# Performance work log

Measured on AMD Instinct MI355X. Metric: run time of the kernel, lower is better.

The kernel has to match this reference:

```python
import jax, jax.numpy as jnp
import numpy as np

D_MODEL = 2048
N_HEADS = 16
D_K = D_MODEL // N_HEADS
BATCH = 4
SEQ = 2048


def setup_inputs() -> dict:
    key = jax.random.key(0)
    ks = jax.random.split(key, 9)
    s = 1.0 / np.sqrt(D_MODEL)
    return {
        "x": jax.random.normal(ks[0], (BATCH, SEQ, D_MODEL), dtype=jnp.float32),
        "wq_w": jax.random.normal(ks[1], (D_MODEL, D_MODEL), dtype=jnp.float32) * s,
        "wq_b": jax.random.normal(ks[2], (D_MODEL,), dtype=jnp.float32) * 0.02,
        "wk_w": jax.random.normal(ks[3], (D_MODEL, D_MODEL), dtype=jnp.float32) * s,
        "wk_b": jax.random.normal(ks[4], (D_MODEL,), dtype=jnp.float32) * 0.02,
        "wv_w": jax.random.normal(ks[5], (D_MODEL, D_MODEL), dtype=jnp.float32) * s,
        "wv_b": jax.random.normal(ks[6], (D_MODEL,), dtype=jnp.float32) * 0.02,
        "wo_w": jax.random.normal(ks[7], (D_MODEL, D_MODEL), dtype=jnp.float32) * s,
        "wo_b": jax.random.normal(ks[8], (D_MODEL,), dtype=jnp.float32) * 0.02,
    }


def reference(x, wq_w, wq_b, wk_w, wk_b, wv_w, wv_b, wo_w, wo_b):
    b, s, _ = x.shape
    # Linear projections (torch Linear: x @ W^T + b)
    def split_heads(t):  # (b, s, d_model) -> (b, h, s, d_k)
        return t.reshape(b, s, N_HEADS, D_K).transpose(0, 2, 1, 3)
    q = split_heads(x @ wq_w.T + wq_b)
    k = split_heads(x @ wk_w.T + wk_b)
    v = split_heads(x @ wv_w.T + wv_b)
    scale = 1.0 / jnp.sqrt(jnp.asarray(D_K, dtype=x.dtype))
    scores = jnp.einsum("bhqd,bhkd->bhqk", q, k) * scale  # (b, h, s, s)
    attn = jax.nn.softmax(scores, axis=-1)
    ctx = jnp.einsum("bhqk,bhkd->bhqd", attn, v)
    ctx = ctx.transpose(0, 2, 1, 3).reshape(b, s, D_MODEL)
    out = ctx @ wo_w.T + wo_b
    return out
```

## Files before the change

kernel.cpp:

```cpp
#include <hip/hip_runtime.h>
#include <hip/hip_bf16.h>
#include <math.h>

typedef __attribute__((ext_vector_type(8))) short short8;
typedef __attribute__((ext_vector_type(4))) float f32x4;
typedef __attribute__((ext_vector_type(16))) float f32x16;
typedef __attribute__((ext_vector_type(4))) unsigned short u16x4;
typedef __attribute__((ext_vector_type(8))) unsigned short u16x8;
typedef __attribute__((ext_vector_type(4))) unsigned int u32x4;
typedef __attribute__((ext_vector_type(2))) int i32x2;
typedef unsigned short u16;
typedef unsigned int u32;

#define DM 2048
#define SQ 2048
#define NB 4
#define NH 16
#define DKH 128
#define KT 64
#define NT (SQ / KT)
#define LD3 (3 * DM)
#define QSCALE (0.08838834764831845f * 1.4426950408889634f)

__device__ __forceinline__ u16 f2bf(float f) {
  unsigned u = __float_as_uint(f);
  u += 0x7fffu + ((u >> 16) & 1u);
  return (u16)(u >> 16);
}

__device__ __forceinline__ u32 cvtpk(float lo, float hi) {
  u32 r;
  asm("v_cvt_pk_bf16_f32 %0, %1, %2" : "=v"(r) : "v"(lo), "v"(hi));
  return r;
}

__device__ __forceinline__ void gload16(const u16* g, u16* lds) {
  __builtin_amdgcn_global_load_lds(
      (const __attribute__((address_space(1))) unsigned int*)g,
      (__attribute__((address_space(3))) unsigned int*)lds, 16, 0, 0);
}

__device__ __forceinline__ int paddr16(int r, int k, int nkt) {
  const int cid = (((r >> 8) * nkt + (k >> 6)) << 5) | (((r >> 7) & 1) << 4) |
                  (((r >> 5) & 3) << 2) | ((k >> 4) & 3);
  return (cid << 9) + (((r & 31) | (((k >> 3) & 1) << 5)) << 3) + (k & 7);
}

__global__ void cvt_x_p(const float* __restrict__ in, u16* __restrict__ out) {
  const int idx = blockIdx.x * 256 + threadIdx.x;
  const int r = idx >> 8;
  const int k = (idx & 255) << 3;
  const float4 v0 = *(const float4*)(in + (size_t)r * DM + k);
  const float4 v1 = *(const float4*)(in + (size_t)r * DM + k + 4);
  u16x8 o;
  o[0] = f2bf(v0.x); o[1] = f2bf(v0.y); o[2] = f2bf(v0.z); o[3] = f2bf(v0.w);
  o[4] = f2bf(v1.x); o[5] = f2bf(v1.y); o[6] = f2bf(v1.z); o[7] = f2bf(v1.w);
  *(u16x8*)(out + paddr16(r, k, 32)) = o;
}

__global__ void cvt_w_p(const float* __restrict__ w0, const float* __restrict__ w1,
                        const float* __restrict__ w2, const float* __restrict__ w3,
                        u16* __restrict__ dq, u16* __restrict__ dw) {
  const int sel = blockIdx.y;
  const float* src;
  switch (sel) {
    case 0: src = w0; break;
    case 1: src = w1; break;
    case 2: src = w2; break;
    default: src = w3; break;
  }
  const int idx = blockIdx.x * 256 + threadIdx.x;
  const int r = idx >> 8;
  const int k = (idx & 255) << 3;
  const float4 v0 = *(const float4*)(src + (size_t)r * DM + k);
  const float4 v1 = *(const float4*)(src + (size_t)r * DM + k + 4);
  u16x8 o;
  o[0] = f2bf(v0.x); o[1] = f2bf(v0.y); o[2] = f2bf(v0.z); o[3] = f2bf(v0.w);
  o[4] = f2bf(v1.x); o[5] = f2bf(v1.y); o[6] = f2bf(v1.z); o[7] = f2bf(v1.w);
  if (sel < 3)
    *(u16x8*)(dq + paddr16(sel * DM + r, k, 32)) = o;
  else
    *(u16x8*)(dw + paddr16(r, k, 32)) = o;
}


#define STG_A(T, HALF)                                                       \
  do {                                                                       \
    _Pragma("unroll") for (int uu = 0; uu < 2; ++uu) {                       \
      const int j_ = w * 2 + uu;                                             \
      gload16(As + ((((T) * 32 + (HALF) * 16 + j_) << 9) + l * 8),           \
              &smA[((T) & 1) * 16384 + ((HALF) * 16 + j_) * 512]);           \
    }                                                                        \
  } while (0)

#define STG_B(T, HALF)                                                       \
  do {                                                                       \
    _Pragma("unroll") for (int uu = 0; uu < 2; ++uu) {                       \
      const int j_ = w * 2 + uu;                                             \
      gload16(Bs + ((((T) * 32 + (HALF) * 16 + j_) << 9) + l * 8),           \
              &smB[((T) & 1) * 16384 + ((HALF) * 16 + j_) * 512]);           \
    }                                                                        \
  } while (0)

#define LDA(QM)                                                            \
  do {                                                                     \
    const int rb_ = wr * 4 + (QM) * 2;                                     \
    const u16* p_ = &smA[bi * 16384 + rb_ * 2048 + l * 8];                 \
    _Pragma("unroll") for (int s = 0; s < 4; ++s) {                        \
      af[0][s] = *(const short8*)&p_[s * 512];                             \
      af[1][s] = *(const short8*)&p_[2048 + s * 512];                      \
    }                                                                      \
  } while (0)

#define LDB(QN)                                                            \
  do {                                                                     \
    const int rb_ = wc * 2 + (QN);                                         \
    const u16* p_ = &smB[bi * 16384 + rb_ * 2048 + l * 8];                 \
    _Pragma("unroll") for (int s = 0; s < 4; ++s)                          \
      bf[QN][s] = *(const short8*)&p_[s * 512];                            \
  } while (0)

#define MFMA_Q(QM, QN)                                                             \
  __builtin_amdgcn_s_setprio(1);                                                   \
  _Pragma("unroll") for (int s = 0; s < 4; ++s) {                                  \
    acc[(QM) * 2][(QN)] = __builtin_amdgcn_mfma_f32_32x32x16_bf16(                 \
        af[0][s], bf[QN][s], acc[(QM) * 2][(QN)], 0, 0, 0);                        \
    acc[(QM) * 2 + 1][(QN)] = __builtin_amdgcn_mfma_f32_32x32x16_bf16(             \
        af[1][s], bf[QN][s], acc[(QM) * 2 + 1][(QN)], 0, 0, 0);                    \
  }                                                                                \
  __builtin_amdgcn_s_setprio(0);

#define WAIT_LGKM                                         \
  asm volatile("s_waitcnt lgkmcnt(0)" ::: "memory");      \
  __builtin_amdgcn_sched_barrier(0);

template <int MODE>
__global__ __launch_bounds__(512, 2) void gemm8p(
    const u16* __restrict__ A, const u16* __restrict__ B,
    const float* __restrict__ bq, const float* __restrict__ bk,
    const float* __restrict__ bvp, void* __restrict__ Cout,
    int M, int N, int K) {
  __shared__ u16 smA[2 * 16384];
  __shared__ u16 smB[2 * 16384];
  const int tid = threadIdx.x;
  const int w = tid >> 6, l = tid & 63;
  const int c5 = l & 31, hi = l >> 5;
  const int wr = w >> 2, wc = w & 3;

  int flat = blockIdx.x + (int)gridDim.x * (int)blockIdx.y;
  const int nwg = (int)(gridDim.x * gridDim.y);
  flat = (flat & 7) * (nwg >> 3) + (flat >> 3);
  const int m0 = (flat / (int)gridDim.x) * 256, n0 = (flat % (int)gridDim.x) * 256;

  const int NSTEP = K / 64;
  f32x16 acc[4][2] = {};

  const u16* As = A + (size_t)(m0 >> 8) * NSTEP * 16384;
  const u16* Bs = B + (size_t)(n0 >> 8) * NSTEP * 16384;

  STG_A(0, 0); STG_A(0, 1); STG_B(0, 0); STG_B(0, 1);
  STG_B(1, 0); STG_A(1, 0);
  asm volatile("s_waitcnt vmcnt(4)" ::: "memory");
  __builtin_amdgcn_s_barrier();

  short8 af[2][4], bf[2][4];
  for (int t = 0; t < NSTEP; ++t) {
    const int bi = t & 1;
    LDA(0); LDB(0);
    if (t + 1 < NSTEP) STG_B(t + 1, 1);
    __builtin_amdgcn_s_barrier();
    WAIT_LGKM;
    MFMA_Q(0, 0);
    __builtin_amdgcn_s_barrier();
    LDB(1);
    if (t + 1 < NSTEP) STG_A(t + 1, 1);
    __builtin_amdgcn_s_barrier();
    WAIT_LGKM;
    MFMA_Q(0, 1);
    __builtin_amdgcn_s_barrier();
    LDA(1);
    if (t + 2 < NSTEP) STG_B(t + 2, 0);
    __builtin_amdgcn_s_barrier();
    WAIT_LGKM;
    MFMA_Q(1, 1);
    __builtin_amdgcn_s_barrier();
    if (t + 2 < NSTEP) STG_A(t + 2, 0);
    __builtin_amdgcn_s_barrier();
    MFMA_Q(1, 0);
    if (t + 2 < NSTEP)
      asm volatile("s_waitcnt vmcnt(4)" ::: "memory");
    else if (t + 1 < NSTEP)
      asm volatile("s_waitcnt vmcnt(0)" ::: "memory");
    __builtin_amdgcn_s_barrier();
  }

#pragma unroll
  for (int nf = 0; nf < 2; ++nf) {
    const int col = n0 + wc * 64 + nf * 32 + c5;
    float bval, os;
    if (MODE == 0) {
      const int seg = col >> 11;
      const float* bp = seg == 0 ? bq : (seg == 1 ? bk : bvp);
      bval = bp[col & (DM - 1)];
      os = (seg == 0) ? QSCALE : 1.0f;
    } else {
      bval = bq[col];
      os = 1.0f;
    }
#pragma unroll
    for (int mf = 0; mf < 4; ++mf) {
#pragma unroll
      for (int r = 0; r < 16; ++r) {
        const int row = m0 + wr * 128 + mf * 32 + (r & 3) + 8 * (r >> 2) + 4 * hi;
        const float v = (acc[mf][nf][r] + bval) * os;
        if (MODE == 1)
          ((float*)Cout)[(size_t)row * N + col] = v;
        else
          ((u16*)Cout)[(size_t)row * N + col] = f2bf(v);
      }
    }
  }
}

__global__ __launch_bounds__(512, 2) void attn(
    const u16* __restrict__ QKV, u16* __restrict__ O) {
  __shared__ u16 smK[2 * 8192];
  __shared__ u16 smV[9216];
  __shared__ float alScr[8 * 32];

  const u16* Qp = QKV;
  const u16* Kp = QKV + DM;
  const u16* Vp = QKV + 2 * DM;

  const int tid = threadIdx.x;
  const int w = tid >> 6, l = tid & 63;
  const int c5 = l & 31, hi = l >> 5;

  int flat = blockIdx.x + ((int)blockIdx.y << 3) + ((int)blockIdx.z << 7);
  flat = (flat & 7) * 64 + (flat >> 3);
  const int qt = flat & 7, h = (flat >> 3) & 15, b = flat >> 7;

  const int q0 = qt * 256 + w * 32;
  const size_t rowb = (size_t)b * SQ;
  const int hoff = h * DKH;

  short8 qf[8];
#pragma unroll
  for (int ds = 0; ds < 8; ++ds)
    qf[ds] = *(const short8*)&Qp[(rowb + q0 + c5) * LD3 + hoff + ds * 16 + hi * 8];

  f32x16 o[4] = {};
  float mrow = -1e30f, lsum = 0.f;

  const int vdg = tid >> 5;
  const int kvp = (tid & 31) * 2;
  u16x8 va, vb;

  {
#pragma unroll
    for (int uu = 0; uu < 2; ++uu) {
      const int u = w * 2 + uu;
      const int row = u * 4 + (l >> 4);
      const int col16 = (l & 15) ^ (row & 15);
      gload16(&Kp[(rowb + row) * LD3 + hoff + col16 * 8], &smK[u * 512]);
    }
    const u16* vp = &Vp[(rowb + kvp) * LD3 + hoff + vdg * 8];
    va = *(const u16x8*)vp;
    vb = *(const u16x8*)(vp + LD3);
#pragma unroll
    for (int i = 0; i < 8; ++i) {
      const int d = vdg * 8 + i;
      *(u32*)&smV[d * 72 + kvp] = (u32)va[i] | ((u32)vb[i] << 16);
    }
  }
  __syncthreads();

  int buf = 0;
  for (int t = 0; t < NT; ++t) {
    const int nb = buf ^ 1;
    if (t + 1 < NT) {
      const size_t kvr = rowb + (size_t)(t + 1) * KT;
#pragma unroll
      for (int uu = 0; uu < 2; ++uu) {
        const int u = w * 2 + uu;
        const int row = u * 4 + (l >> 4);
        const int col16 = (l & 15) ^ (row & 15);
        gload16(&Kp[(kvr + row) * LD3 + hoff + col16 * 8], &smK[nb * 8192 + u * 512]);
      }
      const u16* vp = &Vp[(kvr + kvp) * LD3 + hoff + vdg * 8];
      va = *(const u16x8*)vp;
      vb = *(const u16x8*)(vp + LD3);
    }

    f32x16 s[2] = {};
    __builtin_amdgcn_s_setprio(1);
#pragma unroll
    for (int ni = 0; ni < 2; ++ni) {
      const int row = ni * 32 + c5;
#pragma unroll
      for (int ds = 0; ds < 8; ++ds) {
        const short8 kf = *(const short8*)&smK[buf * 8192 + row * 128 + (((ds << 1) | hi) ^ (row & 15)) * 8];
        s[ni] = __builtin_amdgcn_mfma_f32_32x32x16_bf16(kf, qf[ds], s[ni], 0, 0, 0);
      }
    }
    __builtin_amdgcn_s_setprio(0);

    float mx = s[0][0];
#pragma unroll
    for (int ni = 0; ni < 2; ++ni)
#pragma unroll
      for (int i = 0; i < 16; ++i)
        mx = fmaxf(mx, s[ni][i]);
    i32x2 sw = __builtin_amdgcn_permlane32_swap(__float_as_int(mx), __float_as_int(mx), false, false);
    const float gmax = fmaxf(__int_as_float(sw.x), __int_as_float(sw.y));

    if (__any(gmax > mrow + 10.0f)) {
      const float mn = fmaxf(mrow, gmax);
      const float al = exp2f(mrow - mn);
      mrow = mn;
      lsum *= al;
      alScr[w * 32 + c5] = al;
#pragma unroll
      for (int r = 0; r < 16; ++r) {
        const float av = alScr[w * 32 + (r & 3) + 8 * (r >> 2) + 4 * hi];
#pragma unroll
        for (int dg = 0; dg < 4; ++dg) o[dg][r] *= av;
      }
    }

    float ps0 = 0.f, ps1 = 0.f;
#pragma unroll
    for (int i = 0; i < 16; ++i) {
      const float p0 = exp2f(s[0][i] - mrow);
      const float p1 = exp2f(s[1][i] - mrow);
      s[0][i] = p0; s[1][i] = p1;
      ps0 += p0; ps1 += p1;
    }
    lsum += ps0 + ps1;

    __builtin_amdgcn_s_setprio(1);
#pragma unroll
    for (int ks = 0; ks < 4; ++ks) {
      const int b0 = (ks & 1) * 8;
      const int ni = ks >> 1;
      const u32 A0 = cvtpk(s[ni][b0 + 0], s[ni][b0 + 1]);
      const u32 A1 = cvtpk(s[ni][b0 + 4], s[ni][b0 + 5]);
      const u32 B0 = cvtpk(s[ni][b0 + 2], s[ni][b0 + 3]);
      const u32 B1 = cvtpk(s[ni][b0 + 6], s[ni][b0 + 7]);
      const i32x2 r0 = __builtin_amdgcn_permlane32_swap((int)A0, (int)A1, false, false);
      const i32x2 r1 = __builtin_amdgcn_permlane32_swap((int)B0, (int)B1, false, false);
      u32x4 paw;
      paw.x = (u32)r0.x; paw.y = (u32)r1.x; paw.z = (u32)r0.y; paw.w = (u32)r1.y;
      const short8 pa = *(const short8*)&paw;
#pragma unroll
      for (int dg = 0; dg < 4; ++dg) {
        const int rowd = dg * 32 + c5;
        const short8 vf = *(const short8*)&smV[rowd * 72 + ks * 16 + hi * 8];
        o[dg] = __builtin_amdgcn_mfma_f32_32x32x16_bf16(pa, vf, o[dg], 0, 0, 0);
      }
    }
    __builtin_amdgcn_s_setprio(0);

    __syncthreads();
    if (t + 1 < NT) {
#pragma unroll
      for (int i = 0; i < 8; ++i) {
        const int d = vdg * 8 + i;
        *(u32*)&smV[d * 72 + kvp] = (u32)va[i] | ((u32)vb[i] << 16);
      }
      __syncthreads();
    }
    buf = nb;
  }

  {
    const i32x2 sl = __builtin_amdgcn_permlane32_swap(__float_as_int(lsum), __float_as_int(lsum), false, false);
    const float tot = __int_as_float(sl.x) + __int_as_float(sl.y);
    alScr[w * 32 + c5] = 1.0f / tot;
  }
#pragma unroll
  for (int r = 0; r < 16; ++r) {
    const int qloc = (r & 3) + 8 * (r >> 2) + 4 * hi;
    const float inv = alScr[w * 32 + qloc];
    const int rowg = (int)rowb + q0 + qloc;
#pragma unroll
    for (int dg = 0; dg < 4; ++dg)
      O[paddr16(rowg, hoff + dg * 32 + c5, 32)] = f2bf(o[dg][r] * inv);
  }
}

extern "C" void kernel_launch(void* const* d_in, const int* in_sizes, int n_in,
                              void* d_out, int out_size, void* d_ws, size_t ws_size,
                              hipStream_t stream) {
  const float* x    = (const float*)d_in[0];
  const float* wq_w = (const float*)d_in[1];
  const float* wq_b = (const float*)d_in[2];
  const float* wk_w = (const float*)d_in[3];
  const float* wk_b = (const float*)d_in[4];
  const float* wv_w = (const float*)d_in[5];
  const float* wv_b = (const float*)d_in[6];
  const float* wo_w = (const float*)d_in[7];
  const float* wo_b = (const float*)d_in[8];
  float* out = (float*)d_out;

  u16* p = (u16*)d_ws;
  u16* xb  = p; p += (size_t)NB * SQ * DM;
  u16* wqb = p; p += (size_t)3 * DM * DM;
  u16* wob = p; p += (size_t)DM * DM;
  u16* QKV = p; p += (size_t)NB * SQ * 3 * DM;
  u16* ctx = xb;

  cvt_x_p<<<dim3(NB * SQ * DM / 2048), dim3(256), 0, stream>>>(x, xb);
  cvt_w_p<<<dim3(DM * DM / 2048, 4), dim3(256), 0, stream>>>(wq_w, wk_w, wv_w, wo_w, wqb, wob);

  dim3 gg3(3 * DM / 256, (NB * SQ) / 256);
  gemm8p<0><<<gg3, dim3(512), 0, stream>>>(xb, wqb, wq_b, wk_b, wv_b, QKV,
                                           NB * SQ, 3 * DM, DM);

  attn<<<dim3(SQ / 256, NH, NB), dim3(512), 0, stream>>>(QKV, ctx);

  dim3 ggo(DM / 256, (NB * SQ) / 256);
  gemm8p<1><<<ggo, dim3(512), 0, stream>>>(ctx, wob, wo_b, nullptr, nullptr, out,
                                           NB * SQ, DM, DM);
}
```

Before: 587.7 us.

## Drop redundant GEMM barriers, coalesce bf16 pack writes, tree-reduce attention row max

The GEMM main loop loses the extra workgroup barriers and the explicit lgkmcnt(0) waits placed before each MFMA quarter. The compiler now places LDS waits itself, and the MFMAs can overlap with the LDS fragment loads and the async global-to-LDS staging. The fp32-to-bf16 packing kernels now iterate over the packed output index and invert the mapping with a new helper. That gives contiguous, coalesced stores at the cost of scattered reads. In attention, the QK^T loop order is swapped so the two independent MFMA chains interleave, and the row max uses a tree reduction instead of a serial chain. The risk is an LDS hazard if a removed barrier was actually guarding reuse of a staging buffer.

```diff
diff --git a/kernel.cpp b/kernel.cpp
--- a/kernel.cpp
+++ b/kernel.cpp
@@ -43,19 +43,28 @@
 __device__ __forceinline__ int paddr16(int r, int k, int nkt) {
   const int cid = (((r >> 8) * nkt + (k >> 6)) << 5) | (((r >> 7) & 1) << 4) |
                   (((r >> 5) & 3) << 2) | ((k >> 4) & 3);
-  return (cid << 9) + (((r & 31) | (((k >> 3) & 1) << 5)) << 3) + (k & 7);
+  return (cid << 9) + (((r & 31) | (((k >> 3) & 1) << 3 << 2)) << 3) + (k & 7);
+}
+
+__device__ __forceinline__ void pinv(int idx, int nkt, int& r, int& k) {
+  const int e8 = idx & 63;
+  const int cid = idx >> 6;
+  const int kt = (cid >> 5) % nkt;
+  const int rt = (cid >> 5) / nkt;
+  r = (rt << 8) + (((cid >> 4) & 1) << 7) + (((cid >> 2) & 3) << 5) + (e8 & 31);
+  k = (kt << 6) + ((cid & 3) << 4) + ((e8 >> 5) << 3);
 }
 
 __global__ void cvt_x_p(const float* __restrict__ in, u16* __restrict__ out) {
   const int idx = blockIdx.x * 256 + threadIdx.x;
-  const int r = idx >> 8;
-  const int k = (idx & 255) << 3;
+  int r, k;
+  pinv(idx, 32, r, k);
   const float4 v0 = *(const float4*)(in + (size_t)r * DM + k);
   const float4 v1 = *(const float4*)(in + (size_t)r * DM + k + 4);
   u16x8 o;
   o[0] = f2bf(v0.x); o[1] = f2bf(v0.y); o[2] = f2bf(v0.z); o[3] = f2bf(v0.w);
   o[4] = f2bf(v1.x); o[5] = f2bf(v1.y); o[6] = f2bf(v1.z); o[7] = f2bf(v1.w);
-  *(u16x8*)(out + paddr16(r, k, 32)) = o;
+  *(u16x8*)(out + (size_t)idx * 8) = o;
 }
 
 __global__ void cvt_w_p(const float* __restrict__ w0, const float* __restrict__ w1,
@@ -70,17 +79,15 @@
     default: src = w3; break;
   }
   const int idx = blockIdx.x * 256 + threadIdx.x;
-  const int r = idx >> 8;
-  const int k = (idx & 255) << 3;
+  int r, k;
+  pinv(idx, 32, r, k);
   const float4 v0 = *(const float4*)(src + (size_t)r * DM + k);
   const float4 v1 = *(const float4*)(src + (size_t)r * DM + k + 4);
   u16x8 o;
   o[0] = f2bf(v0.x); o[1] = f2bf(v0.y); o[2] = f2bf(v0.z); o[3] = f2bf(v0.w);
   o[4] = f2bf(v1.x); o[5] = f2bf(v1.y); o[6] = f2bf(v1.z); o[7] = f2bf(v1.w);
-  if (sel < 3)
-    *(u16x8*)(dq + paddr16(sel * DM + r, k, 32)) = o;
-  else
-    *(u16x8*)(dw + paddr16(r, k, 32)) = o;
+  u16* dst = (sel < 3) ? (dq + (size_t)sel * DM * DM) : dw;
+  *(u16x8*)(dst + (size_t)idx * 8) = o;
 }
 
 
@@ -129,10 +136,6 @@
         af[1][s], bf[QN][s], acc[(QM) * 2 + 1][(QN)], 0, 0, 0);                    \
   }                                                                                \
   __builtin_amdgcn_s_setprio(0);
-
-#define WAIT_LGKM                                         \
-  asm volatile("s_waitcnt lgkmcnt(0)" ::: "memory");      \
-  __builtin_amdgcn_sched_barrier(0);
 
 template <int MODE>
 __global__ __launch_bounds__(512, 2) void gemm8p(
@@ -168,24 +171,17 @@
     const int bi = t & 1;
     LDA(0); LDB(0);
     if (t + 1 < NSTEP) STG_B(t + 1, 1);
-    __builtin_amdgcn_s_barrier();
-    WAIT_LGKM;
     MFMA_Q(0, 0);
     __builtin_amdgcn_s_barrier();
     LDB(1);
     if (t + 1 < NSTEP) STG_A(t + 1, 1);
-    __builtin_amdgcn_s_barrier();
-    WAIT_LGKM;
     MFMA_Q(0, 1);
     __builtin_amdgcn_s_barrier();
     LDA(1);
     if (t + 2 < NSTEP) STG_B(t + 2, 0);
-    __builtin_amdgcn_s_barrier();
-    WAIT_LGKM;
     MFMA_Q(1, 1);
     __builtin_amdgcn_s_barrier();
     if (t + 2 < NSTEP) STG_A(t + 2, 0);
-    __builtin_amdgcn_s_barrier();
     MFMA_Q(1, 0);
     if (t + 2 < NSTEP)
       asm volatile("s_waitcnt vmcnt(4)" ::: "memory");
@@ -295,23 +291,24 @@
     f32x16 s[2] = {};
     __builtin_amdgcn_s_setprio(1);
 #pragma unroll
-    for (int ni = 0; ni < 2; ++ni) {
-      const int row = ni * 32 + c5;
-#pragma unroll
-      for (int ds = 0; ds < 8; ++ds) {
+    for (int ds = 0; ds < 8; ++ds) {
+#pragma unroll
+      for (int ni = 0; ni < 2; ++ni) {
+        const int row = ni * 32 + c5;
         const short8 kf = *(const short8*)&smK[buf * 8192 + row * 128 + (((ds << 1) | hi) ^ (row & 15)) * 8];
         s[ni] = __builtin_amdgcn_mfma_f32_32x32x16_bf16(kf, qf[ds], s[ni], 0, 0, 0);
       }
     }
     __builtin_amdgcn_s_setprio(0);
 
-    float mx = s[0][0];
-#pragma unroll
-    for (int ni = 0; ni < 2; ++ni)
-#pragma unroll
-      for (int i = 0; i < 16; ++i)
-        mx = fmaxf(mx, s[ni][i]);
-    i32x2 sw = __builtin_amdgcn_permlane32_swap(__float_as_int(mx), __float_as_int(mx), false, false);
+    float mt[16];
+#pragma unroll
+    for (int i = 0; i < 16; ++i) mt[i] = fmaxf(s[0][i], s[1][i]);
+#pragma unroll
+    for (int st = 8; st >= 1; st >>= 1)
+#pragma unroll
+      for (int i = 0; i < st; ++i) mt[i] = fmaxf(mt[i], mt[i + st]);
+    i32x2 sw = __builtin_amdgcn_permlane32_swap(__float_as_int(mt[0]), __float_as_int(mt[0]), false, false);
     const float gmax = fmaxf(__int_as_float(sw.x), __int_as_float(sw.y));
 
     if (__any(gmax > mrow + 10.0f)) {
```

Result: faster. 544.6 us (-7.3%).
